# Performance work log

Hardware: AMD Instinct MI355X
Metric: run time of the kernel (lower is better)

The kernel has to match this reference:

```python
import jax, jax.numpy as jnp
import numpy as np

B, N, NH, E_IN = 2, 2048, 32, 128   # batch, grid cells, neighborhood size, input feat
MD, H, FF, OUT = 512, 8, 2048, 128  # model_dim, heads, ff_dim, output_dim
HD = MD // H                        # head dim = 64
PED, TABLE = 32, 512                # pos_emb_dim, number of (distance,phi) bins
EPS = 1e-5


def setup_inputs() -> dict:
    key = jax.random.key(0)
    ks = jax.random.split(key, 16)
    def w(k, shp, s=0.02):
        return jax.random.normal(k, shp, jnp.float32) * s
    return {
        "x": jax.random.normal(ks[0], (B, N, NH, E_IN), jnp.float32),
        "distances": jax.random.randint(ks[1], (B * N, NH, NH), 0, TABLE),
        "phis": jax.random.randint(ks[2], (B * N, NH, NH), 0, TABLE),
        "W_in": w(ks[3], (E_IN, MD)),
        "dist_table": w(ks[4], (TABLE, PED), 1.0),
        "phi_table": w(ks[5], (TABLE, PED), 1.0),
        "W_bias": w(ks[6], (PED, H)),
        "Wq": w(ks[7], (MD, MD)),
        "Wk": w(ks[8], (MD, MD)),
        "Wv": w(ks[9], (MD, MD)),
        "Wo": w(ks[10], (MD, MD)),
        "W_ff1": w(ks[11], (MD, FF)),
        "W_ff2": w(ks[12], (FF, MD)),
        "g1": jnp.ones((MD,), jnp.float32),
        "b1": jnp.zeros((MD,), jnp.float32),
        "g2": jnp.ones((MD,), jnp.float32),
        "b2": jnp.zeros((MD,), jnp.float32),
        "W_out": w(ks[13], (MD, OUT)),
    }


def _layernorm(x, g, b):
    m = x.mean(-1, keepdims=True)
    v = ((x - m) ** 2).mean(-1, keepdims=True)
    return (x - m) * jax.lax.rsqrt(v + EPS) * g + b


def reference(x, distances, phis, W_in, dist_table, phi_table, W_bias,
              Wq, Wk, Wv, Wo, W_ff1, W_ff2, g1, b1, g2, b2, W_out):
    b, n, nh, _ = x.shape
    m = b * n
    # input_mlp (bias-free Linear), fold (b, n) into batch of attention problems
    h = (x @ W_in).reshape(m, nh, MD)                       # [m, nh, MD]
    # relative position bias: emb_table lookup, product, Linear(PED -> H)
    pe = dist_table[distances] * phi_table[phis]            # [m, nh, nh, PED]
    bias = jnp.einsum('mijp,ph->mhij', pe, W_bias)          # [m, H, nh, nh]
    # MHA with qkv projections (bias-free)
    q = (h @ Wq).reshape(m, nh, H, HD).transpose(0, 2, 1, 3)
    k = (h @ Wk).reshape(m, nh, H, HD).transpose(0, 2, 1, 3)
    v = (h @ Wv).reshape(m, nh, H, HD).transpose(0, 2, 1, 3)
    scores = jnp.einsum('mhid,mhjd->mhij', q, k) / np.sqrt(HD).astype(np.float32)
    att = jax.nn.softmax(scores + bias, axis=-1)            # [m, H, nh, nh]
    o = jnp.einsum('mhij,mhjd->mhid', att, v)
    att_out = o.transpose(0, 2, 1, 3).reshape(m, nh, MD) @ Wo
    # q_res residual (dropout=0), LayerNorm, FFN (SiLU), LayerNorm
    h1 = _layernorm(h + att_out, g1, b1)
    ff = jax.nn.silu(h1 @ W_ff1) @ W_ff2
    h2 = _layernorm(h1 + ff, g2, b2)
    # unfold and output_mlp
    return h2.reshape(b, n, nh, MD) @ W_out                 # [b, n, nh, OUT]
```

## Files before the change

kernel.cpp:

```cpp
#include <hip/hip_runtime.h>
#include <hip/hip_bf16.h>
#include <cstdint>
#include <cstddef>

typedef __bf16 bf16;
typedef __bf16 bf16x8 __attribute__((ext_vector_type(8)));
typedef float  f32x4  __attribute__((ext_vector_type(4)));
typedef float  f32x16 __attribute__((ext_vector_type(16)));

#define DEVI static __device__ __forceinline__

DEVI void gload_lds16(const void* g, void* l) {
  __builtin_amdgcn_global_load_lds(
      (const __attribute__((address_space(1))) uint32_t*)(uintptr_t)g,
      (__attribute__((address_space(3))) uint32_t*)(uint32_t)(uintptr_t)l,
      16, 0, 0);
}

DEVI float ldf(const void* p, size_t i, bool isbf) {
  return isbf ? (float)((const bf16*)p)[i] : ((const float*)p)[i];
}

__global__ void probe_dtype(const void* w, int* flag) {
  int tid = threadIdx.x;
  const bf16* p = (const bf16*)w;
  float mx = 0.f;
  for (int i = tid; i < 2048; i += 64) {
    float v = fabsf((float)p[i]);
    if (!(v < 1e30f)) v = 1e30f;
    mx = fmaxf(mx, v);
  }
#pragma unroll
  for (int d = 32; d; d >>= 1) mx = fmaxf(mx, __shfl_xor(mx, d, 64));
  if (tid == 0) *flag = (mx < 100.f) ? 1 : 0;
}

__global__ void convert_bf16(const void* src, size_t eoff, bf16* dst, int n,
                             const int* flag) {
  int i = (blockIdx.x * 256 + threadIdx.x) * 8;
  if (i >= n) return;
  if (*flag) {
    *(uint4*)(dst + i) = *(const uint4*)((const bf16*)src + eoff + i);
  } else {
    const float* s = (const float*)src + eoff + i;
    float4 a = *(const float4*)s;
    float4 b = *(const float4*)(s + 4);
    bf16 o[8] = {(bf16)a.x, (bf16)a.y, (bf16)a.z, (bf16)a.w,
                 (bf16)b.x, (bf16)b.y, (bf16)b.z, (bf16)b.w};
    *(uint4*)(dst + i) = *(const uint4*)o;
  }
}

__global__ void convert_f32(const void* src, float* dst, int n, const int* flag) {
  int i = blockIdx.x * 256 + threadIdx.x;
  if (i >= n) return;
  dst[i] = ldf(src, i, *flag != 0);
}

__global__ void transpose_w(const void* W, bf16* WT, int K, int N, const int* flag) {
  int idx = blockIdx.x * 256 + threadIdx.x;
  if (idx >= K * N) return;
  int n = idx / K, k = idx - n * K;
  WT[idx] = (bf16)ldf(W, (size_t)k * N + n, *flag != 0);
}

__global__ __launch_bounds__(256) void build_F(const float* __restrict__ dt32,
                                               const float* __restrict__ pt32,
                                               const float* __restrict__ Wb32,
                                               bf16* __restrict__ F) {
  __shared__ float WbS[256];
  WbS[threadIdx.x] = Wb32[threadIdx.x];
  __syncthreads();
  int pair = blockIdx.x * 256 + threadIdx.x;
  int d = pair >> 9, ph = pair & 511;
  const float4* dtv = (const float4*)(dt32 + (size_t)d * 32);
  const float4* ptv = (const float4*)(pt32 + (size_t)ph * 32);
  float acc[8] = {0, 0, 0, 0, 0, 0, 0, 0};
#pragma unroll
  for (int q = 0; q < 8; ++q) {
    float4 a = dtv[q], b = ptv[q];
    float pe[4] = {a.x * b.x, a.y * b.y, a.z * b.z, a.w * b.w};
#pragma unroll
    for (int e = 0; e < 4; ++e)
#pragma unroll
      for (int hh = 0; hh < 8; ++hh) acc[hh] += pe[e] * WbS[(q * 4 + e) * 8 + hh];
  }
  bf16 o[8];
#pragma unroll
  for (int hh = 0; hh < 8; ++hh) o[hh] = (bf16)acc[hh];
  *(uint4*)(F + (size_t)pair * 8) = *(const uint4*)o;
}

__global__ __launch_bounds__(256) void build_bias(const int* __restrict__ dist,
                                                  const int* __restrict__ phi,
                                                  const bf16* __restrict__ F,
                                                  bf16* __restrict__ bias) {
  const int m = blockIdx.x;
#pragma unroll
  for (int it = 0; it < 4; ++it) {
    int e = it * 256 + threadIdx.x;
    int d = dist[(size_t)m * 1024 + e];
    int ph = phi[(size_t)m * 1024 + e];
    uint4 fv = *(const uint4*)(F + ((size_t)d * 512 + ph) * 8);
    const bf16* fe = (const bf16*)&fv;
#pragma unroll
    for (int hh = 0; hh < 8; ++hh)
      bias[((size_t)m * 8 + hh) * 1024 + e] = fe[hh];
  }
}

template <int DO_SILU, int OUT_DUAL>
__global__ __launch_bounds__(256) void gemm_bt(const bf16* __restrict__ A,
                                               const bf16* __restrict__ BT,
                                               void* __restrict__ Cv, int N, int K,
                                               const int* flag, size_t row0) {
  __shared__ bf16 As[128 * 32];
  __shared__ bf16 Bs[128 * 32];
  const int bn = blockIdx.x * 128;
  const int bm = blockIdx.y * 128;
  const int tid = threadIdx.x;
  const int lane = tid & 63;
  const int wave = tid >> 6;
  const int wr = (wave >> 1) * 64, wc = (wave & 1) * 64;
  const int srow = tid >> 2, skk = (tid & 3) * 8;
  const size_t sK = (size_t)K;
  const int kq = (lane >> 4) * 8;
  const int fr = lane & 15;
  f32x4 acc[4][4] = {};
  for (int k0 = 0; k0 < K; k0 += 32) {
    __syncthreads();
    gload_lds16(A + (size_t)(bm + srow) * sK + k0 + skk, As + tid * 8);
    gload_lds16(A + (size_t)(bm + 64 + srow) * sK + k0 + skk, As + 2048 + tid * 8);
    gload_lds16(BT + (size_t)(bn + srow) * sK + k0 + skk, Bs + tid * 8);
    gload_lds16(BT + (size_t)(bn + 64 + srow) * sK + k0 + skk, Bs + 2048 + tid * 8);
    __syncthreads();
    bf16x8 af[4], bfr[4];
#pragma unroll
    for (int i = 0; i < 4; ++i)
      af[i] = *(const bf16x8*)(As + (wr + i * 16 + fr) * 32 + kq);
#pragma unroll
    for (int j = 0; j < 4; ++j)
      bfr[j] = *(const bf16x8*)(Bs + (wc + j * 16 + fr) * 32 + kq);
#pragma unroll
    for (int i = 0; i < 4; ++i)
#pragma unroll
      for (int j = 0; j < 4; ++j)
        acc[i][j] = __builtin_amdgcn_mfma_f32_16x16x32_bf16(af[i], bfr[j], acc[i][j], 0, 0, 0);
  }
  const int fq = (lane >> 4) * 4;
  const bool write_f32 = OUT_DUAL && flag && (*flag == 0);
#pragma unroll
  for (int i = 0; i < 4; ++i)
#pragma unroll
    for (int j = 0; j < 4; ++j)
#pragma unroll
      for (int r = 0; r < 4; ++r) {
        size_t row = row0 + (size_t)(bm + wr + i * 16 + fq + r);
        size_t col = (size_t)(bn + wc + j * 16 + fr);
        float v = acc[i][j][r];
        if (DO_SILU) v = v / (1.f + __expf(-v));
        if (OUT_DUAL && write_f32)
          ((float*)Cv)[row * N + col] = v;
        else
          ((bf16*)Cv)[row * N + col] = (bf16)v;
      }
}

__global__ __launch_bounds__(512) void attn_fused(const bf16* __restrict__ QKV,
                                                  const bf16* __restrict__ bias,
                                                  bf16* __restrict__ O) {
  const int m = blockIdx.x;
  const int lane = threadIdx.x & 63;
  const int h = threadIdx.x >> 6;
  __shared__ bf16 Vs[8][32 * 64];
  __shared__ bf16 Ps[8][32 * 32];
  const size_t rowbase = (size_t)m * 32 * 1536;
#pragma unroll
  for (int rr = 0; rr < 4; ++rr) {
    int e = rr * 512 + lane * 8;
    int i = e >> 6, c = e & 63;
    *(uint4*)&Vs[h][e] =
        *(const uint4*)(QKV + rowbase + (size_t)i * 1536 + 1024 + h * 64 + c);
  }
  const int fr = lane & 31;
  const int kq = (lane >> 5) * 8;
  bf16x8 qf[4], kf[4];
#pragma unroll
  for (int kk = 0; kk < 4; ++kk) {
    qf[kk] = *(const bf16x8*)(QKV + rowbase + (size_t)fr * 1536 + h * 64 + kk * 16 + kq);
    kf[kk] = *(const bf16x8*)(QKV + rowbase + (size_t)fr * 1536 + 512 + h * 64 + kk * 16 + kq);
  }
  f32x16 s = {};
#pragma unroll
  for (int kk = 0; kk < 4; ++kk)
    s = __builtin_amdgcn_mfma_f32_32x32x16_bf16(qf[kk], kf[kk], s, 0, 0, 0);
  const bf16* bp = bias + ((size_t)m * 8 + h) * 1024;
  const int ri = 4 * (lane >> 5);
  float p[16];
#pragma unroll
  for (int r = 0; r < 16; ++r) {
    int i = (r & 3) + 8 * (r >> 2) + ri;
    p[r] = s[r] * 0.125f + (float)bp[i * 32 + fr];
  }
#pragma unroll
  for (int r = 0; r < 16; ++r) {
    float mx = p[r];
#pragma unroll
    for (int d = 16; d; d >>= 1) mx = fmaxf(mx, __shfl_xor(mx, d, 64));
    float e = __expf(p[r] - mx);
    float sum = e;
#pragma unroll
    for (int d = 16; d; d >>= 1) sum += __shfl_xor(sum, d, 64);
    p[r] = e / sum;
  }
#pragma unroll
  for (int r = 0; r < 16; ++r) {
    int i = (r & 3) + 8 * (r >> 2) + ri;
    Ps[h][i * 32 + fr] = (bf16)p[r];
  }
  __syncthreads();
  bf16x8 pf[2];
#pragma unroll
  for (int kk = 0; kk < 2; ++kk)
    pf[kk] = *(const bf16x8*)(&Ps[h][fr * 32 + kk * 16 + kq]);
  f32x16 o0 = {}, o1 = {};
#pragma unroll
  for (int kk = 0; kk < 2; ++kk) {
    bf16x8 v0, v1;
#pragma unroll
    for (int e = 0; e < 8; ++e) {
      v0[e] = Vs[h][(kk * 16 + kq + e) * 64 + fr];
      v1[e] = Vs[h][(kk * 16 + kq + e) * 64 + 32 + fr];
    }
    o0 = __builtin_amdgcn_mfma_f32_32x32x16_bf16(pf[kk], v0, o0, 0, 0, 0);
    o1 = __builtin_amdgcn_mfma_f32_32x32x16_bf16(pf[kk], v1, o1, 0, 0, 0);
  }
  bf16* op = O + (size_t)m * 32 * 512 + h * 64;
#pragma unroll
  for (int r = 0; r < 16; ++r) {
    int i = (r & 3) + 8 * (r >> 2) + ri;
    op[(size_t)i * 512 + fr] = (bf16)o0[r];
    op[(size_t)i * 512 + 32 + fr] = (bf16)o1[r];
  }
}

__global__ __launch_bounds__(256) void ln_fused(const bf16* __restrict__ X,
                                                const bf16* __restrict__ Y,
                                                const bf16* __restrict__ gb, int gboff,
                                                bf16* __restrict__ out) {
  const int row = blockIdx.x * 4 + (threadIdx.x >> 6);
  const int lane = threadIdx.x & 63;
  uint4 xr = *(const uint4*)(X + (size_t)row * 512 + lane * 8);
  uint4 yr = *(const uint4*)(Y + (size_t)row * 512 + lane * 8);
  const bf16* xe = (const bf16*)&xr;
  const bf16* ye = (const bf16*)&yr;
  float v[8];
  float sum = 0.f;
#pragma unroll
  for (int e = 0; e < 8; ++e) { v[e] = (float)xe[e] + (float)ye[e]; sum += v[e]; }
#pragma unroll
  for (int d = 32; d; d >>= 1) sum += __shfl_xor(sum, d, 64);
  float mean = sum * (1.f / 512.f);
  float var = 0.f;
#pragma unroll
  for (int e = 0; e < 8; ++e) { float t = v[e] - mean; var += t * t; }
#pragma unroll
  for (int d = 32; d; d >>= 1) var += __shfl_xor(var, d, 64);
  float rstd = rsqrtf(var * (1.f / 512.f) + 1e-5f);
  uint4 gr = *(const uint4*)(gb + gboff + lane * 8);
  uint4 br = *(const uint4*)(gb + gboff + 512 + lane * 8);
  const bf16* ge = (const bf16*)&gr;
  const bf16* be = (const bf16*)&br;
  bf16 o[8];
#pragma unroll
  for (int e = 0; e < 8; ++e)
    o[e] = (bf16)((v[e] - mean) * rstd * (float)ge[e] + (float)be[e]);
  *(uint4*)(out + (size_t)row * 512 + lane * 8) = *(const uint4*)o;
}

extern "C" void kernel_launch(void* const* d_in, const int* in_sizes, int n_in,
                              void* d_out, int out_size, void* d_ws, size_t ws_size,
                              hipStream_t stream) {
  const int T = 131072;
  const void* x    = d_in[0];
  const int*  dist = (const int*)d_in[1];
  const int*  phiI = (const int*)d_in[2];
  const void* Win  = d_in[3];
  const void* dtab = d_in[4];
  const void* ptab = d_in[5];
  const void* Wb   = d_in[6];
  const void* Wq   = d_in[7];
  const void* Wk   = d_in[8];
  const void* Wv   = d_in[9];
  const void* Wo   = d_in[10];
  const void* Wf1  = d_in[11];
  const void* Wf2  = d_in[12];
  const void* g1   = d_in[13];
  const void* b1   = d_in[14];
  const void* g2   = d_in[15];
  const void* b2   = d_in[16];
  const void* Wout = d_in[17];
  (void)in_sizes; (void)n_in; (void)out_size;

  const size_t FIXED = (size_t)16 << 20;
  int R = 131072;
  while (R > 1024 && FIXED + (size_t)R * 7936 > ws_size) R >>= 1;
  const int MC = R / 32;
  const int NCHUNK = T / R;

  char* wsb = (char*)d_ws;
  size_t off = 0;
  auto alloc = [&](size_t bytes) {
    char* p = wsb + off;
    off += (bytes + 511) & ~(size_t)511;
    return p;
  };
  int*  flag = (int*)alloc(4);
  bf16* gb   = (bf16*)alloc(2048 * 2);
  float* dt32 = (float*)alloc((size_t)512 * 32 * 4);
  float* pt32 = (float*)alloc((size_t)512 * 32 * 4);
  float* Wb32 = (float*)alloc(256 * 4);
  bf16* WinT = (bf16*)alloc((size_t)512 * 128 * 2);
  bf16* QKVT = (bf16*)alloc((size_t)1536 * 512 * 2);
  bf16* WoT  = (bf16*)alloc((size_t)512 * 512 * 2);
  bf16* Wf1T = (bf16*)alloc((size_t)2048 * 512 * 2);
  bf16* Wf2T = (bf16*)alloc((size_t)512 * 2048 * 2);
  bf16* WouT = (bf16*)alloc((size_t)128 * 512 * 2);
  bf16* Ftab = (bf16*)alloc((size_t)262144 * 8 * 2);
  bf16* Xc   = (bf16*)alloc((size_t)R * 128 * 2);
  bf16* Hc   = (bf16*)alloc((size_t)R * 512 * 2);
  bf16* big  = (bf16*)alloc((size_t)R * 2048 * 2);
  bf16* Oc   = (bf16*)alloc((size_t)R * 512 * 2);
  bf16* AOc  = (bf16*)alloc((size_t)R * 512 * 2);
  bf16* biasc= (bf16*)alloc((size_t)MC * 8 * 1024 * 2);

  probe_dtype<<<1, 64, 0, stream>>>(Win, flag);
  convert_bf16<<<1, 256, 0, stream>>>(g1, 0, gb + 0, 512, flag);
  convert_bf16<<<1, 256, 0, stream>>>(b1, 0, gb + 512, 512, flag);
  convert_bf16<<<1, 256, 0, stream>>>(g2, 0, gb + 1024, 512, flag);
  convert_bf16<<<1, 256, 0, stream>>>(b2, 0, gb + 1536, 512, flag);
  convert_f32<<<64, 256, 0, stream>>>(dtab, dt32, 512 * 32, flag);
  convert_f32<<<64, 256, 0, stream>>>(ptab, pt32, 512 * 32, flag);
  convert_f32<<<1, 256, 0, stream>>>(Wb, Wb32, 256, flag);
  transpose_w<<<(512 * 128 + 255) / 256, 256, 0, stream>>>(Win, WinT, 128, 512, flag);
  transpose_w<<<(512 * 512 + 255) / 256, 256, 0, stream>>>(Wq, QKVT, 512, 512, flag);
  transpose_w<<<(512 * 512 + 255) / 256, 256, 0, stream>>>(Wk, QKVT + 512 * 512, 512, 512, flag);
  transpose_w<<<(512 * 512 + 255) / 256, 256, 0, stream>>>(Wv, QKVT + 1024 * 512, 512, 512, flag);
  transpose_w<<<(512 * 512 + 255) / 256, 256, 0, stream>>>(Wo, WoT, 512, 512, flag);
  transpose_w<<<(2048 * 512 + 255) / 256, 256, 0, stream>>>(Wf1, Wf1T, 512, 2048, flag);
  transpose_w<<<(2048 * 512 + 255) / 256, 256, 0, stream>>>(Wf2, Wf2T, 2048, 512, flag);
  transpose_w<<<(128 * 512 + 255) / 256, 256, 0, stream>>>(Wout, WouT, 512, 128, flag);
  build_F<<<262144 / 256, 256, 0, stream>>>(dt32, pt32, Wb32, Ftab);

  dim3 blk(256);
  for (int c = 0; c < NCHUNK; ++c) {
    const size_t rowoff = (size_t)c * R;
    const size_t moff = (size_t)c * MC;
    convert_bf16<<<(R * 128 / 8 + 255) / 256, 256, 0, stream>>>(x, rowoff * 128, Xc, R * 128, flag);
    gemm_bt<0, 0><<<dim3(4, R / 128), blk, 0, stream>>>(Xc, WinT, Hc, 512, 128, nullptr, 0);
    gemm_bt<0, 0><<<dim3(12, R / 128), blk, 0, stream>>>(Hc, QKVT, big, 1536, 512, nullptr, 0);
    build_bias<<<MC, 256, 0, stream>>>(dist + moff * 1024, phiI + moff * 1024, Ftab, biasc);
    attn_fused<<<MC, 512, 0, stream>>>(big, biasc, Oc);
    gemm_bt<0, 0><<<dim3(4, R / 128), blk, 0, stream>>>(Oc, WoT, AOc, 512, 512, nullptr, 0);
    ln_fused<<<R / 4, 256, 0, stream>>>(Hc, AOc, gb, 0, Hc);
    gemm_bt<1, 0><<<dim3(16, R / 128), blk, 0, stream>>>(Hc, Wf1T, big, 2048, 512, nullptr, 0);
    gemm_bt<0, 0><<<dim3(4, R / 128), blk, 0, stream>>>(big, Wf2T, AOc, 512, 2048, nullptr, 0);
    ln_fused<<<R / 4, 256, 0, stream>>>(Hc, AOc, gb, 1024, Hc);
    gemm_bt<0, 1><<<dim3(1, R / 128), blk, 0, stream>>>(Hc, WouT, d_out, 128, 512, flag, rowoff);
  }
}
```

Baseline: 2.216 ms.

## Fuse bias gather into attention, fold input conversion into GEMM, widen K step

```diff
diff --git a/kernel.cpp b/kernel.cpp
--- a/kernel.cpp
+++ b/kernel.cpp
@@ -91,61 +91,86 @@
   *(uint4*)(F + (size_t)pair * 8) = *(const uint4*)o;
 }
 
-__global__ __launch_bounds__(256) void build_bias(const int* __restrict__ dist,
-                                                  const int* __restrict__ phi,
-                                                  const bf16* __restrict__ F,
-                                                  bf16* __restrict__ bias) {
-  const int m = blockIdx.x;
-#pragma unroll
-  for (int it = 0; it < 4; ++it) {
-    int e = it * 256 + threadIdx.x;
-    int d = dist[(size_t)m * 1024 + e];
-    int ph = phi[(size_t)m * 1024 + e];
-    uint4 fv = *(const uint4*)(F + ((size_t)d * 512 + ph) * 8);
-    const bf16* fe = (const bf16*)&fv;
-#pragma unroll
-    for (int hh = 0; hh < 8; ++hh)
-      bias[((size_t)m * 8 + hh) * 1024 + e] = fe[hh];
-  }
-}
-
-template <int DO_SILU, int OUT_DUAL>
-__global__ __launch_bounds__(256) void gemm_bt(const bf16* __restrict__ A,
+template <int DO_SILU, int OUT_DUAL, int A_CONV>
+__global__ __launch_bounds__(256) void gemm_bt(const void* __restrict__ Av,
+                                               size_t aoff,
                                                const bf16* __restrict__ BT,
                                                void* __restrict__ Cv, int N, int K,
                                                const int* flag, size_t row0) {
-  __shared__ bf16 As[128 * 32];
-  __shared__ bf16 Bs[128 * 32];
+  __shared__ bf16 As[2][128 * 32];
+  __shared__ bf16 Bs[2][128 * 32];
   const int bn = blockIdx.x * 128;
   const int bm = blockIdx.y * 128;
   const int tid = threadIdx.x;
   const int lane = tid & 63;
   const int wave = tid >> 6;
   const int wr = (wave >> 1) * 64, wc = (wave & 1) * 64;
-  const int srow = tid >> 2, skk = (tid & 3) * 8;
+  const int srow = tid >> 2;
+  const int scol = (tid & 3) * 8;
   const size_t sK = (size_t)K;
   const int kq = (lane >> 4) * 8;
   const int fr = lane & 15;
+  const bf16* A = (const bf16*)Av + (A_CONV ? 0 : aoff);
+  const bool a_isbf = A_CONV ? (*flag != 0) : true;
   f32x4 acc[4][4] = {};
-  for (int k0 = 0; k0 < K; k0 += 32) {
+  for (int k0 = 0; k0 < K; k0 += 64) {
+    bf16x8 aval[2][2];
+    if (A_CONV) {
+#pragma unroll
+      for (int h = 0; h < 2; ++h)
+#pragma unroll
+        for (int p = 0; p < 2; ++p) {
+          size_t eidx = aoff + (size_t)(bm + p * 64 + srow) * sK + k0 + h * 32 + scol;
+          if (a_isbf) {
+            aval[h][p] = *(const bf16x8*)((const bf16*)Av + eidx);
+          } else {
+            const float* s = (const float*)Av + eidx;
+            float4 a = *(const float4*)s;
+            float4 b = *(const float4*)(s + 4);
+            bf16x8 o;
+            o[0] = (bf16)a.x; o[1] = (bf16)a.y; o[2] = (bf16)a.z; o[3] = (bf16)a.w;
+            o[4] = (bf16)b.x; o[5] = (bf16)b.y; o[6] = (bf16)b.z; o[7] = (bf16)b.w;
+            aval[h][p] = o;
+          }
+        }
+    }
     __syncthreads();
-    gload_lds16(A + (size_t)(bm + srow) * sK + k0 + skk, As + tid * 8);
-    gload_lds16(A + (size_t)(bm + 64 + srow) * sK + k0 + skk, As + 2048 + tid * 8);
-    gload_lds16(BT + (size_t)(bn + srow) * sK + k0 + skk, Bs + tid * 8);
-    gload_lds16(BT + (size_t)(bn + 64 + srow) * sK + k0 + skk, Bs + 2048 + tid * 8);
+    if (A_CONV) {
+#pragma unroll
+      for (int h = 0; h < 2; ++h)
+#pragma unroll
+        for (int p = 0; p < 2; ++p)
+          *(bf16x8*)(&As[h][(p * 64 + srow) * 32 + scol]) = aval[h][p];
+    } else {
+#pragma unroll
+      for (int h = 0; h < 2; ++h)
+#pragma unroll
+        for (int p = 0; p < 2; ++p)
+          gload_lds16(A + (size_t)(bm + p * 64 + srow) * sK + k0 + h * 32 + scol,
+                      &As[h][p * 2048] + (tid & 255) * 8);
+    }
+#pragma unroll
+    for (int h = 0; h < 2; ++h)
+#pragma unroll
+      for (int p = 0; p < 2; ++p)
+        gload_lds16(BT + (size_t)(bn + p * 64 + srow) * sK + k0 + h * 32 + scol,
+                    &Bs[h][p * 2048] + (tid & 255) * 8);
     __syncthreads();
-    bf16x8 af[4], bfr[4];
-#pragma unroll
-    for (int i = 0; i < 4; ++i)
-      af[i] = *(const bf16x8*)(As + (wr + i * 16 + fr) * 32 + kq);
-#pragma unroll
-    for (int j = 0; j < 4; ++j)
-      bfr[j] = *(const bf16x8*)(Bs + (wc + j * 16 + fr) * 32 + kq);
-#pragma unroll
-    for (int i = 0; i < 4; ++i)
+#pragma unroll
+    for (int kh = 0; kh < 2; ++kh) {
+      bf16x8 af[4], bfr[4];
+#pragma unroll
+      for (int i = 0; i < 4; ++i)
+        af[i] = *(const bf16x8*)(&As[kh][(wr + i * 16 + fr) * 32 + kq]);
 #pragma unroll
       for (int j = 0; j < 4; ++j)
-        acc[i][j] = __builtin_amdgcn_mfma_f32_16x16x32_bf16(af[i], bfr[j], acc[i][j], 0, 0, 0);
+        bfr[j] = *(const bf16x8*)(&Bs[kh][(wc + j * 16 + fr) * 32 + kq]);
+#pragma unroll
+      for (int i = 0; i < 4; ++i)
+#pragma unroll
+        for (int j = 0; j < 4; ++j)
+          acc[i][j] = __builtin_amdgcn_mfma_f32_16x16x32_bf16(af[i], bfr[j], acc[i][j], 0, 0, 0);
+    }
   }
   const int fq = (lane >> 4) * 4;
   const bool write_f32 = OUT_DUAL && flag && (*flag == 0);
@@ -167,7 +192,9 @@
 }
 
 __global__ __launch_bounds__(512) void attn_fused(const bf16* __restrict__ QKV,
-                                                  const bf16* __restrict__ bias,
+                                                  const int* __restrict__ dist,
+                                                  const int* __restrict__ phi,
+                                                  const bf16* __restrict__ F,
                                                   bf16* __restrict__ O) {
   const int m = blockIdx.x;
   const int lane = threadIdx.x & 63;
@@ -194,13 +221,17 @@
 #pragma unroll
   for (int kk = 0; kk < 4; ++kk)
     s = __builtin_amdgcn_mfma_f32_32x32x16_bf16(qf[kk], kf[kk], s, 0, 0, 0);
-  const bf16* bp = bias + ((size_t)m * 8 + h) * 1024;
+  const int* dmp = dist + (size_t)m * 1024;
+  const int* pmp = phi + (size_t)m * 1024;
   const int ri = 4 * (lane >> 5);
   float p[16];
 #pragma unroll
   for (int r = 0; r < 16; ++r) {
     int i = (r & 3) + 8 * (r >> 2) + ri;
-    p[r] = s[r] * 0.125f + (float)bp[i * 32 + fr];
+    int e = i * 32 + fr;
+    int d = dmp[e], ph = pmp[e];
+    float bias = (float)F[((size_t)d * 512 + ph) * 8 + h];
+    p[r] = s[r] * 0.125f + bias;
   }
 #pragma unroll
   for (int r = 0; r < 16; ++r) {
@@ -304,7 +335,7 @@
 
   const size_t FIXED = (size_t)16 << 20;
   int R = 131072;
-  while (R > 1024 && FIXED + (size_t)R * 7936 > ws_size) R >>= 1;
+  while (R > 1024 && FIXED + (size_t)R * 7168 > ws_size) R >>= 1;
   const int MC = R / 32;
   const int NCHUNK = T / R;
 
@@ -327,12 +358,10 @@
   bf16* Wf2T = (bf16*)alloc((size_t)512 * 2048 * 2);
   bf16* WouT = (bf16*)alloc((size_t)128 * 512 * 2);
   bf16* Ftab = (bf16*)alloc((size_t)262144 * 8 * 2);
-  bf16* Xc   = (bf16*)alloc((size_t)R * 128 * 2);
   bf16* Hc   = (bf16*)alloc((size_t)R * 512 * 2);
   bf16* big  = (bf16*)alloc((size_t)R * 2048 * 2);
   bf16* Oc   = (bf16*)alloc((size_t)R * 512 * 2);
   bf16* AOc  = (bf16*)alloc((size_t)R * 512 * 2);
-  bf16* biasc= (bf16*)alloc((size_t)MC * 8 * 1024 * 2);
 
   probe_dtype<<<1, 64, 0, stream>>>(Win, flag);
   convert_bf16<<<1, 256, 0, stream>>>(g1, 0, gb + 0, 512, flag);
@@ -356,16 +385,21 @@
   for (int c = 0; c < NCHUNK; ++c) {
     const size_t rowoff = (size_t)c * R;
     const size_t moff = (size_t)c * MC;
-    convert_bf16<<<(R * 128 / 8 + 255) / 256, 256, 0, stream>>>(x, rowoff * 128, Xc, R * 128, flag);
-    gemm_bt<0, 0><<<dim3(4, R / 128), blk, 0, stream>>>(Xc, WinT, Hc, 512, 128, nullptr, 0);
-    gemm_bt<0, 0><<<dim3(12, R / 128), blk, 0, stream>>>(Hc, QKVT, big, 1536, 512, nullptr, 0);
-    build_bias<<<MC, 256, 0, stream>>>(dist + moff * 1024, phiI + moff * 1024, Ftab, biasc);
-    attn_fused<<<MC, 512, 0, stream>>>(big, biasc, Oc);
-    gemm_bt<0, 0><<<dim3(4, R / 128), blk, 0, stream>>>(Oc, WoT, AOc, 512, 512, nullptr, 0);
+    gemm_bt<0, 0, 1><<<dim3(4, R / 128), blk, 0, stream>>>(
+        x, rowoff * 128, WinT, Hc, 512, 128, flag, 0);
+    gemm_bt<0, 0, 0><<<dim3(12, R / 128), blk, 0, stream>>>(
+        Hc, 0, QKVT, big, 1536, 512, nullptr, 0);
+    attn_fused<<<MC, 512, 0, stream>>>(big, dist + moff * 1024, phiI + moff * 1024,
+                                       Ftab, Oc);
+    gemm_bt<0, 0, 0><<<dim3(4, R / 128), blk, 0, stream>>>(
+        Oc, 0, WoT, AOc, 512, 512, nullptr, 0);
     ln_fused<<<R / 4, 256, 0, stream>>>(Hc, AOc, gb, 0, Hc);
-    gemm_bt<1, 0><<<dim3(16, R / 128), blk, 0, stream>>>(Hc, Wf1T, big, 2048, 512, nullptr, 0);
-    gemm_bt<0, 0><<<dim3(4, R / 128), blk, 0, stream>>>(big, Wf2T, AOc, 512, 2048, nullptr, 0);
+    gemm_bt<1, 0, 0><<<dim3(16, R / 128), blk, 0, stream>>>(
+        Hc, 0, Wf1T, big, 2048, 512, nullptr, 0);
+    gemm_bt<0, 0, 0><<<dim3(4, R / 128), blk, 0, stream>>>(
+        big, 0, Wf2T, AOc, 512, 2048, nullptr, 0);
     ln_fused<<<R / 4, 256, 0, stream>>>(Hc, AOc, gb, 1024, Hc);
-    gemm_bt<0, 1><<<dim3(1, R / 128), blk, 0, stream>>>(Hc, WouT, d_out, 128, 512, flag, rowoff);
-  }
-}
+    gemm_bt<0, 1, 0><<<dim3(1, R / 128), blk, 0, stream>>>(
+        Hc, 0, WouT, d_out, 128, 512, flag, rowoff);
+  }
+}
```

New measurement: 1.956 ms. -11.8%, faster.
